# Kernel optimization log

Hardware: AMD Instinct MI355X
Metric: run time of the kernel (lower is better)

Reference implementation:

```python
import jax, jax.numpy as jnp
import numpy as np

D_MODEL = 528
N_HEADS = 16
FEAT = 16           # feature_dim
HEAD_DIM = 33       # d_model // num_heads == 2*FEAT + 1 (required by the module's math)
WINDOW = 64
EPS = 1e-9


def setup_inputs() -> dict:
    key = jax.random.key(0)
    ks = jax.random.split(key, 10)
    B, S = 2, 2048
    hidden_states = jax.random.normal(ks[0], (B, S, D_MODEL), dtype=jnp.float32)
    attention_mask = jnp.ones((B, S), dtype=jnp.int32)
    sc = 0.02
    # weights stored as (in, out); torch Linear applies x @ W.T so this is the transposed weight
    Wq_lin = jax.random.normal(ks[1], (D_MODEL, FEAT * N_HEADS), dtype=jnp.float32) * sc
    Wk_lin = jax.random.normal(ks[2], (D_MODEL, FEAT * N_HEADS), dtype=jnp.float32) * sc
    Wv_lin = jax.random.normal(ks[3], (D_MODEL, HEAD_DIM * N_HEADS), dtype=jnp.float32) * sc
    Wo_lin = jax.random.normal(ks[4], (HEAD_DIM * N_HEADS, D_MODEL), dtype=jnp.float32) * sc
    Wq_win = jax.random.normal(ks[5], (D_MODEL, D_MODEL), dtype=jnp.float32) * sc
    Wk_win = jax.random.normal(ks[6], (D_MODEL, D_MODEL), dtype=jnp.float32) * sc
    Wv_win = jax.random.normal(ks[7], (D_MODEL, D_MODEL), dtype=jnp.float32) * sc
    Wo_win = jax.random.normal(ks[8], (D_MODEL, D_MODEL), dtype=jnp.float32) * sc
    return {
        "hidden_states": hidden_states,
        "attention_mask": attention_mask,
        "Wq_lin": Wq_lin, "Wk_lin": Wk_lin, "Wv_lin": Wv_lin, "Wo_lin": Wo_lin,
        "Wq_win": Wq_win, "Wk_win": Wk_win, "Wv_win": Wv_win, "Wo_win": Wo_win,
    }


def _linear_attention(x, mask, Wq, Wk, Wv, Wo):
    B, S, _ = x.shape
    q = (x @ Wq).reshape(B, S, N_HEADS, FEAT).transpose(0, 2, 1, 3)      # bhsf
    k = (x @ Wk).reshape(B, S, N_HEADS, FEAT).transpose(0, 2, 1, 3)
    v = (x @ Wv).reshape(B, S, N_HEADS, HEAD_DIM).transpose(0, 2, 1, 3)  # bhse
    # Taylor feature map: [1, q, 0.5*q^2] -> feature dim 2*FEAT+1 == HEAD_DIM
    qe = jnp.concatenate([jnp.ones_like(q[..., :1]), q, 0.5 * q * q], axis=-1)
    ke = jnp.concatenate([jnp.ones_like(k[..., :1]), k, 0.5 * k * k], axis=-1)
    kv = jnp.einsum('bhnd,bhne->bhde', ke, v)          # (B,H,Dexp,HEAD_DIM)
    qkv = jnp.einsum('bhnd,bhde->bhne', qe, kv)        # (B,H,S,HEAD_DIM)
    # z[b,h,n,e] = (sum_d qe[b,h,n,d]) * ksum[b,h,e]  (faithful to torch einsum with size-1 n)
    z = qe.sum(-1, keepdims=True) * ke.sum(2, keepdims=True)  # (B,H,S,Dexp==HEAD_DIM)
    out = qkv / (z + EPS)
    out = jnp.where((mask == 0)[:, None, :, None], 0.0, out)
    out = out.transpose(0, 2, 1, 3).reshape(B, S, N_HEADS * HEAD_DIM)
    return out @ Wo


def _window_attention(x, mask, Wq, Wk, Wv, Wo):
    B, S, _ = x.shape
    q = (x @ Wq).reshape(B, S, N_HEADS, HEAD_DIM).transpose(0, 2, 1, 3)
    k = (x @ Wk).reshape(B, S, N_HEADS, HEAD_DIM).transpose(0, 2, 1, 3)
    v = (x @ Wv).reshape(B, S, N_HEADS, HEAD_DIM).transpose(0, 2, 1, 3)
    scores = jnp.einsum('bhnd,bhmd->bhnm', q, k) / np.sqrt(HEAD_DIM).astype(np.float32)
    # tril(diagonal=window_size-1): allow key index m <= n + WINDOW - 1
    i = jnp.arange(S)[:, None]
    j = jnp.arange(S)[None, :]
    band = (j <= i + WINDOW - 1)
    neg_inf = jnp.asarray(-jnp.inf, scores.dtype)
    scores = jnp.where(band[None, None], scores, neg_inf)
    scores = jnp.where((mask == 0)[:, None, None, :], neg_inf, scores)
    attn = jax.nn.softmax(scores, axis=-1)
    out = jnp.einsum('bhnm,bhmd->bhnd', attn, v)
    out = out.transpose(0, 2, 1, 3).reshape(B, S, D_MODEL)
    return out @ Wo


def reference(hidden_states, attention_mask,
              Wq_lin, Wk_lin, Wv_lin, Wo_lin,
              Wq_win, Wk_win, Wv_win, Wo_win):
    lin = _linear_attention(hidden_states, attention_mask, Wq_lin, Wk_lin, Wv_lin, Wo_lin)
    win = _window_attention(hidden_states, attention_mask, Wq_win, Wk_win, Wv_win, Wo_win)
    return lin + win
```

## Files before the change

kernel.cpp:

```cpp
#include <hip/hip_runtime.h>

#define NH 16
#define FEAT 16
#define HD 33
#define DM 528
#define WIN 64
#define EPSF 1e-9f
#define K1C (0.17407765595569785f * 1.4426950408889634f)
#define KP 544
#define KSPLIT 1632
#define NPROJ 2112
#define KOUT 1056
#define OPS 4352
#define NCH 16
#define ZPARTS 4

typedef float f32x4 __attribute__((ext_vector_type(4)));
typedef short short8 __attribute__((ext_vector_type(8)));

__device__ inline ushort f2bf(float f) {
  uint u = __float_as_uint(f);
  uint r = u + 0x7fffu + ((u >> 16) & 1u);
  return (ushort)(r >> 16);
}
__device__ inline ushort f2bf_tr(float f) { return (ushort)(__float_as_uint(f) >> 16); }
__device__ inline float bf2f(ushort u) { return __uint_as_float(((uint)u) << 16); }

__global__ __launch_bounds__(256) void prep_all(const float* __restrict__ x,
                                                const float* __restrict__ Wq_lin,
                                                const float* __restrict__ Wk_lin,
                                                const float* __restrict__ Wv_lin,
                                                const float* __restrict__ Wo_lin,
                                                const float* __restrict__ Wq_win,
                                                const float* __restrict__ Wk_win,
                                                const float* __restrict__ Wv_win,
                                                const float* __restrict__ Wo_win,
                                                ushort* __restrict__ xhi,
                                                ushort* __restrict__ xlo,
                                                ushort* __restrict__ Wqks,
                                                ushort* __restrict__ WprojT,
                                                ushort* __restrict__ WoT2, int M) {
  const int stride = gridDim.x * 256;
  const int tid0 = blockIdx.x * 256 + threadIdx.x;
  for (int j = tid0; j < M * 68; j += stride) {
    int row = j / 68, c8 = (j - row * 68) * 8;
    short8 h8, l8;
    if (c8 < DM) {
      float4 f0 = *(const float4*)&x[(size_t)row * DM + c8];
      float4 f1 = *(const float4*)&x[(size_t)row * DM + c8 + 4];
      float vv[8] = {f0.x, f0.y, f0.z, f0.w, f1.x, f1.y, f1.z, f1.w};
#pragma unroll
      for (int z = 0; z < 8; ++z) {
        ushort h = f2bf(vv[z]);
        h8[z] = (short)h;
        l8[z] = (short)f2bf(vv[z] - bf2f(h));
      }
    } else {
      h8 = (short8){0, 0, 0, 0, 0, 0, 0, 0};
      l8 = h8;
    }
    *(short8*)&xhi[(size_t)row * KP + c8] = h8;
    *(short8*)&xlo[(size_t)row * KP + c8] = l8;
  }
  for (int i = tid0; i < 512 * KSPLIT; i += stride) {
    int n = i / KSPLIT, kp = i - n * KSPLIT;
    int seg = kp / KP, kk = kp - seg * KP;
    float v = 0.f;
    if (kk < DM) v = (n < 256) ? Wq_lin[(size_t)kk * 256 + n] : Wk_lin[(size_t)kk * 256 + (n - 256)];
    ushort h = f2bf(v);
    if (seg == 2) h = f2bf(v - bf2f(h));
    Wqks[i] = h;
  }
  for (int i = tid0; i < NPROJ * KP; i += stride) {
    int n = i / KP, k = i - n * KP;
    float v = 0.f;
    if (k < DM) {
      if (n < DM) v = Wq_win[(size_t)k * DM + n];
      else if (n < 2 * DM) v = Wk_win[(size_t)k * DM + (n - DM)] * K1C;
      else if (n < 3 * DM) v = Wv_win[(size_t)k * DM + (n - 2 * DM)];
      else v = Wv_lin[(size_t)k * DM + (n - 3 * DM)];
    }
    WprojT[i] = f2bf(v);
  }
  for (int i = tid0; i < DM * KOUT; i += stride) {
    int n = i / KOUT, k = i - n * KOUT;
    float v = (k < DM) ? Wo_lin[(size_t)k * DM + n] : Wo_win[(size_t)(k - DM) * DM + n];
    WoT2[i] = f2bf(v);
  }
}

__global__ __launch_bounds__(256) void proj_fused(const ushort* __restrict__ xhi,
                                                  const ushort* __restrict__ xlo,
                                                  const ushort* __restrict__ Wqks,
                                                  const ushort* __restrict__ WprojT,
                                                  float* __restrict__ qk,
                                                  ushort* __restrict__ qkvw,
                                                  float* __restrict__ v_lin,
                                                  const int* __restrict__ maskp,
                                                  int S) {
  __shared__ ushort As[128][36];
  __shared__ ushort Bs[128][36];
  const int bm = blockIdx.x * 128;
  const int tid = threadIdx.x;
  const int lane = tid & 63, w = tid >> 6;
  const int lo = lane & 15, hi = lane >> 4;
  const int wr = w >> 1, wc = w & 1;
  const short8 zv = {0, 0, 0, 0, 0, 0, 0, 0};
  f32x4 acc[4][4];
#pragma unroll
  for (int mb = 0; mb < 4; ++mb)
#pragma unroll
    for (int nb = 0; nb < 4; ++nb) acc[mb][nb] = (f32x4){0.f, 0.f, 0.f, 0.f};

  if (blockIdx.y < 17) {
    const int bn = blockIdx.y * 128;
    for (int k0 = 0; k0 < KP; k0 += 32) {
      short8 a_ld[2], b_ld[2];
#pragma unroll
      for (int p = 0; p < 2; ++p) {
        int c = tid + p * 256;
        int row = c >> 2, cc = c & 3;
        a_ld[p] = *(const short8*)&xhi[(size_t)(bm + row) * KP + k0 + cc * 8];
        int bnr = bn + row;
        b_ld[p] = (bnr < NPROJ) ? *(const short8*)&WprojT[(size_t)bnr * KP + k0 + cc * 8] : zv;
      }
      __syncthreads();
#pragma unroll
      for (int p = 0; p < 2; ++p) {
        int c = tid + p * 256;
        int row = c >> 2, cc = c & 3;
        *(short8*)&As[row][cc * 8] = a_ld[p];
        *(short8*)&Bs[row][cc * 8] = b_ld[p];
      }
      __syncthreads();
      short8 afr[4], bfr[4];
#pragma unroll
      for (int mb = 0; mb < 4; ++mb) afr[mb] = *(const short8*)&As[wr * 64 + 16 * mb + lo][8 * hi];
#pragma unroll
      for (int nb = 0; nb < 4; ++nb) bfr[nb] = *(const short8*)&Bs[wc * 64 + 16 * nb + lo][8 * hi];
#pragma unroll
      for (int mb = 0; mb < 4; ++mb)
#pragma unroll
        for (int nb = 0; nb < 4; ++nb)
          acc[mb][nb] = __builtin_amdgcn_mfma_f32_16x16x32_bf16(afr[mb], bfr[nb], acc[mb][nb], 0, 0, 0);
    }
#pragma unroll
    for (int nb = 0; nb < 4; ++nb) {
      const int col = bn + wc * 64 + 16 * nb + lo;
      if (col >= NPROJ) continue;
      const int seg = col / DM;
      const int cc = col - seg * DM;
      if (seg == 3) {
#pragma unroll
        for (int mb = 0; mb < 4; ++mb)
#pragma unroll
          for (int r = 0; r < 4; ++r) {
            int row = bm + wr * 64 + 16 * mb + 4 * hi + r;
            v_lin[(size_t)row * DM + cc] = acc[mb][nb][r];
          }
      } else {
        const uint h = ((uint)cc * 993u) >> 15;
        const int e = cc - (int)h * 33;
        ushort* dst = qkvw + (size_t)seg * (32u * (uint)S * 40u);
#pragma unroll
        for (int mb = 0; mb < 4; ++mb)
#pragma unroll
          for (int r = 0; r < 4; ++r) {
            int row = bm + wr * 64 + 16 * mb + 4 * hi + r;
            int b = (row >= S) ? 1 : 0;
            int nn = row - b * S;
            float val = acc[mb][nb][r];
            if (seg == 2) {
              size_t tb = (size_t)(b * NH + (int)h) * 40;
              dst[(tb + e) * S + nn] = f2bf(val);
              if (e == 0) {
                dst[(tb + 33) * S + nn] = 0x3F80;
#pragma unroll
                for (int z = 34; z < 40; ++z) dst[(tb + z) * S + nn] = 0;
              }
            } else {
              size_t base = ((size_t)(b * NH + (int)h) * S + nn) * 40;
              dst[base + e] = f2bf(val);
              if (e == 0) {
                ushort pad33 = (seg == 0) ? (ushort)0x3F80
                                          : (maskp[row] ? (ushort)0 : f2bf(-1e30f));
                dst[base + 33] = pad33;
#pragma unroll
                for (int z = 34; z < 40; ++z) dst[base + z] = 0;
              }
            }
          }
      }
    }
  } else {
    const int bn = (blockIdx.y - 17) * 128;
    for (int k0 = 0; k0 < KSPLIT; k0 += 32) {
      const int seg = k0 / KP;
      const int kk = k0 - seg * KP;
      const ushort* xsrc = (seg == 1) ? xlo : xhi;
      short8 a_ld[2], b_ld[2];
#pragma unroll
      for (int p = 0; p < 2; ++p) {
        int c = tid + p * 256;
        int row = c >> 2, cc = c & 3;
        a_ld[p] = *(const short8*)&xsrc[(size_t)(bm + row) * KP + kk + cc * 8];
        b_ld[p] = *(const short8*)&Wqks[(size_t)(bn + row) * KSPLIT + k0 + cc * 8];
      }
      __syncthreads();
#pragma unroll
      for (int p = 0; p < 2; ++p) {
        int c = tid + p * 256;
        int row = c >> 2, cc = c & 3;
        *(short8*)&As[row][cc * 8] = a_ld[p];
        *(short8*)&Bs[row][cc * 8] = b_ld[p];
      }
      __syncthreads();
      short8 afr[4], bfr[4];
#pragma unroll
      for (int mb = 0; mb < 4; ++mb) afr[mb] = *(const short8*)&As[wr * 64 + 16 * mb + lo][8 * hi];
#pragma unroll
      for (int nb = 0; nb < 4; ++nb) bfr[nb] = *(const short8*)&Bs[wc * 64 + 16 * nb + lo][8 * hi];
#pragma unroll
      for (int mb = 0; mb < 4; ++mb)
#pragma unroll
        for (int nb = 0; nb < 4; ++nb)
          acc[mb][nb] = __builtin_amdgcn_mfma_f32_16x16x32_bf16(afr[mb], bfr[nb], acc[mb][nb], 0, 0, 0);
    }
#pragma unroll
    for (int mb = 0; mb < 4; ++mb)
#pragma unroll
      for (int nb = 0; nb < 4; ++nb) {
        int col = bn + wc * 64 + 16 * nb + lo;
#pragma unroll
        for (int r = 0; r < 4; ++r) {
          int row = bm + wr * 64 + 16 * mb + 4 * hi + r;
          qk[(size_t)row * 512 + col] = acc[mb][nb][r];
        }
      }
  }
}

__global__ __launch_bounds__(256) void gemm_out(const ushort* __restrict__ A,
                                                const ushort* __restrict__ Bt,
                                                float* __restrict__ C, int S) {
  __shared__ ushort As[128][36];
  __shared__ ushort Bs[128][36];
  const int bm = blockIdx.x * 128, bn = blockIdx.y * 128;
  const int tid = threadIdx.x;
  const int lane = tid & 63, w = tid >> 6;
  const int lo = lane & 15, hi = lane >> 4;
  const int wr = w >> 1, wc = w & 1;
  f32x4 acc[4][4];
#pragma unroll
  for (int mb = 0; mb < 4; ++mb)
#pragma unroll
    for (int nb = 0; nb < 4; ++nb) acc[mb][nb] = (f32x4){0.f, 0.f, 0.f, 0.f};
  const short8 zv = {0, 0, 0, 0, 0, 0, 0, 0};

  for (int k0 = 0; k0 < KOUT; k0 += 32) {
    short8 a_ld[2], b_ld[2];
#pragma unroll
    for (int p = 0; p < 2; ++p) {
      int c = tid + p * 256;
      int row = c >> 2, cc = c & 3;
      a_ld[p] = *(const short8*)&A[(size_t)(bm + row) * KOUT + k0 + cc * 8];
      int bnr = bn + row;
      b_ld[p] = (bnr < DM) ? *(const short8*)&Bt[(size_t)bnr * KOUT + k0 + cc * 8] : zv;
    }
    __syncthreads();
#pragma unroll
    for (int p = 0; p < 2; ++p) {
      int c = tid + p * 256;
      int row = c >> 2, cc = c & 3;
      *(short8*)&As[row][cc * 8] = a_ld[p];
      *(short8*)&Bs[row][cc * 8] = b_ld[p];
    }
    __syncthreads();
    short8 afr[4], bfr[4];
#pragma unroll
    for (int mb = 0; mb < 4; ++mb) afr[mb] = *(const short8*)&As[wr * 64 + 16 * mb + lo][8 * hi];
#pragma unroll
    for (int nb = 0; nb < 4; ++nb) bfr[nb] = *(const short8*)&Bs[wc * 64 + 16 * nb + lo][8 * hi];
#pragma unroll
    for (int mb = 0; mb < 4; ++mb)
#pragma unroll
      for (int nb = 0; nb < 4; ++nb)
        acc[mb][nb] = __builtin_amdgcn_mfma_f32_16x16x32_bf16(afr[mb], bfr[nb], acc[mb][nb], 0, 0, 0);
  }
#pragma unroll
  for (int nb = 0; nb < 4; ++nb) {
    const int col = bn + wc * 64 + 16 * nb + lo;
    if (col >= DM) continue;
#pragma unroll
    for (int mb = 0; mb < 4; ++mb)
#pragma unroll
      for (int r = 0; r < 4; ++r) {
        int row = bm + wr * 64 + 16 * mb + 4 * hi + r;
        C[(size_t)row * DM + col] = acc[mb][nb][r];
      }
  }
}

__global__ __launch_bounds__(256) void lin_kv_part(const float* __restrict__ qk,
                                                   const float* __restrict__ v_lin,
                                                   float* __restrict__ kvp,
                                                   int B, int S) {
  const int bh = blockIdx.x, chunk = blockIdx.y;
  const int b = bh >> 4, h = bh & 15;
  const int tid = threadIdx.x;
  __shared__ float kraw[64][17];
  __shared__ float vsh[64][36];
  if (tid < 64) { vsh[tid][33] = 1.f; vsh[tid][34] = 0.f; vsh[tid][35] = 0.f; }
  f32x4 acc0 = {0.f, 0.f, 0.f, 0.f}, acc1 = {0.f, 0.f, 0.f, 0.f};
  const int d0 = tid / 9, c40 = (tid % 9) * 4;
  const int idx1 = tid + 256;
  const int d1 = idx1 / 9, c41 = (idx1 % 9) * 4;
  const int SC = S / NCH;
  const int nbeg = chunk * SC;
  __syncthreads();
  for (int n0 = nbeg; n0 < nbeg + SC; n0 += 64) {
    {
      int row = tid >> 2, f4 = (tid & 3) * 4;
      float4 kv4 = *(const float4*)&qk[(size_t)(b * S + n0 + row) * 512 + 256 + h * 16 + f4];
      kraw[row][f4 + 0] = kv4.x; kraw[row][f4 + 1] = kv4.y;
      kraw[row][f4 + 2] = kv4.z; kraw[row][f4 + 3] = kv4.w;
    }
    for (int i = tid; i < 64 * 33; i += 256) {
      int n = i / 33, e = i - n * 33;
      vsh[n][e] = v_lin[(size_t)(b * S + n0 + n) * DM + h * HD + e];
    }
    __syncthreads();
#pragma unroll 4
    for (int n = 0; n < 64; ++n) {
      {
        float ke;
        if (d0 == 0) ke = 1.f;
        else if (d0 < 17) ke = kraw[n][d0 - 1];
        else { float kk = kraw[n][d0 - 17]; ke = 0.5f * kk * kk; }
        f32x4 v = *(const f32x4*)&vsh[n][c40];
        acc0 += ke * v;
      }
      if (idx1 < 297) {
        float ke;
        if (d1 < 17) ke = kraw[n][d1 - 1];
        else { float kk = kraw[n][d1 - 17]; ke = 0.5f * kk * kk; }
        f32x4 v = *(const f32x4*)&vsh[n][c41];
        acc1 += ke * v;
      }
    }
    __syncthreads();
  }
  float* dst = kvp + (size_t)(bh * NCH + chunk) * 1188;
  *(f32x4*)&dst[d0 * 36 + c40] = acc0;
  if (idx1 < 297) *(f32x4*)&dst[d1 * 36 + c41] = acc1;
}

__global__ __launch_bounds__(256) void lin_red(const float* __restrict__ kvp,
                                               float* __restrict__ kvr) {
  int bh = blockIdx.x;
  for (int i = threadIdx.x; i < 1188; i += 256) {
    float s = 0.f;
#pragma unroll
    for (int c = 0; c < NCH; ++c) s += kvp[(size_t)(bh * NCH + c) * 1188 + i];
    kvr[(size_t)bh * 1188 + i] = s;
  }
}

__global__ __launch_bounds__(256) void win_lin(const ushort* __restrict__ qwb,
                                               const ushort* __restrict__ kwb,
                                               const ushort* __restrict__ vwbT,
                                               ushort* __restrict__ Opart,
                                               const float* __restrict__ qk,
                                               const float* __restrict__ kvr,
                                               const int* __restrict__ mask,
                                               ushort* __restrict__ cat,
                                               int B, int S, int NT2) {
  __shared__ ushort Ps[4][32][72];
  const int tid = threadIdx.x;
  const int NWINBLK = NT2 * 32 * ZPARTS;
  const int bx = blockIdx.x;

  if (bx < NWINBLK) {
    const int part = bx / (NT2 * 32);
    const int rem = bx - part * (NT2 * 32);
    const int bh = rem / NT2;
    const int qt = NT2 - 1 - (rem - bh * NT2);
    const int NT = NT2 * 2;
    const int T = min(NT, 2 * qt + 3);
    if (part >= T) return;
    const int n0 = qt * 128;
    const int lane = tid & 63, w = tid >> 6;
    const int lo = lane & 15, hi = lane >> 4;
    const short8 zv = {0, 0, 0, 0, 0, 0, 0, 0};

    short8 qf[2][2];
#pragma unroll
    for (int qr = 0; qr < 2; ++qr) {
      const ushort* qrow = qwb + ((size_t)bh * S + n0 + w * 32 + qr * 16 + lo) * 40;
      qf[qr][0] = *(const short8*)&qrow[8 * hi];
      qf[qr][1] = (hi == 0) ? *(const short8*)&qrow[32] : zv;
    }

    const ushort* kb = kwb + (size_t)bh * S * 40;
    const ushort* vb = vwbT + (size_t)bh * 40 * S;
    int evc[3];
#pragma unroll
    for (int eb = 0; eb < 3; ++eb) {
      int e = 16 * eb + lo;
      evc[eb] = (e > 39) ? 39 : e;
    }

    f32x4 Oacc[2][3];
#pragma unroll
    for (int qr = 0; qr < 2; ++qr)
#pragma unroll
      for (int eb = 0; eb < 3; ++eb) Oacc[qr][eb] = (f32x4){0.f, 0.f, 0.f, 0.f};

    for (int t = part; t < T; t += ZPARTS) {
      const int m0 = t * 64;
      short8 kf0[4], kf1[4];
#pragma unroll
      for (int bb = 0; bb < 4; ++bb) {
        const ushort* kr = kb + (size_t)(m0 + 16 * bb + lo) * 40;
        kf0[bb] = *(const short8*)&kr[8 * hi];
        kf1[bb] = *(const short8*)&kr[32];
      }
      short8 vf0[3], vf1[3];
#pragma unroll
      for (int eb = 0; eb < 3; ++eb) {
        const ushort* vr = vb + (size_t)evc[eb] * S + m0;
        vf0[eb] = *(const short8*)&vr[8 * hi];
        vf1[eb] = *(const short8*)&vr[32 + 8 * hi];
      }

      f32x4 accS[2][4];
#pragma unroll
      for (int qr = 0; qr < 2; ++qr)
#pragma unroll
        for (int bb = 0; bb < 4; ++bb) accS[qr][bb] = (f32x4){0.f, 0.f, 0.f, 0.f};
      __builtin_amdgcn_s_setprio(1);
#pragma unroll
      for (int bb = 0; bb < 4; ++bb)
#pragma unroll
        for (int qr = 0; qr < 2; ++qr) {
          accS[qr][bb] = __builtin_amdgcn_mfma_f32_16x16x32_bf16(qf[qr][0], kf0[bb], accS[qr][bb], 0, 0, 0);
          accS[qr][bb] = __builtin_amdgcn_mfma_f32_16x16x32_bf16(qf[qr][1], kf1[bb], accS[qr][bb], 0, 0, 0);
        }
      __builtin_amdgcn_s_setprio(0);

      const bool boundary = (m0 > n0);
      const int dmn = m0 - n0;
#pragma unroll
      for (int qr = 0; qr < 2; ++qr)
#pragma unroll
        for (int bb = 0; bb < 4; ++bb)
#pragma unroll
          for (int r = 0; r < 4; ++r) {
            float p = exp2f(accS[qr][bb][r]);
            if (boundary) {
              int rr = w * 32 + qr * 16 + 4 * hi + r;
              int c = 16 * bb + lo;
              if (c > rr + 63 - dmn) p = 0.f;
            }
            Ps[w][qr * 16 + 4 * hi + r][16 * bb + lo] = f2bf_tr(p);
          }

      __builtin_amdgcn_s_setprio(1);
#pragma unroll
      for (int qr = 0; qr < 2; ++qr) {
        short8 pf0 = *(const short8*)&Ps[w][qr * 16 + lo][8 * hi];
        short8 pf1 = *(const short8*)&Ps[w][qr * 16 + lo][32 + 8 * hi];
#pragma unroll
        for (int eb = 0; eb < 3; ++eb) {
          Oacc[qr][eb] = __builtin_amdgcn_mfma_f32_16x16x32_bf16(pf0, vf0[eb], Oacc[qr][eb], 0, 0, 0);
          Oacc[qr][eb] = __builtin_amdgcn_mfma_f32_16x16x32_bf16(pf1, vf1[eb], Oacc[qr][eb], 0, 0, 0);
        }
      }
      __builtin_amdgcn_s_setprio(0);
    }

    const size_t ob = ((size_t)(bh * NT2 + qt) * ZPARTS + part) * OPS;
#pragma unroll
    for (int qr = 0; qr < 2; ++qr)
#pragma unroll
      for (int eb = 0; eb < 3; ++eb) {
        int e = 16 * eb + lo;
        if (e < 34) {
#pragma unroll
          for (int r = 0; r < 4; ++r)
            Opart[ob + (size_t)(w * 32 + qr * 16 + 4 * hi + r) * 34 + e] = f2bf(Oacc[qr][eb][r]);
        }
      }
  } else {
    const int bs = bx - NWINBLK;
    const int b = (bs >= S) ? 1 : 0;
    float* qsh = (float*)Ps;
    for (int i = tid; i < NH * FEAT; i += 256)
      qsh[(i >> 4) * 17 + (i & 15)] = qk[(size_t)bs * 512 + i];
    __syncthreads();
    const int msk = mask[bs];
    for (int o = tid; o < DM; o += 256) {
      uint h = ((uint)o * 993u) >> 15;
      int e = o - (int)h * 33;
      const float* kvh = kvr + (size_t)(b * NH + (int)h) * 1188;
      float qsum = 1.f, qkv = kvh[e];
#pragma unroll
      for (int f = 0; f < FEAT; ++f) {
        float q = qsh[h * 17 + f];
        float q2 = 0.5f * q * q;
        qsum += q + q2;
        qkv += q * kvh[(1 + f) * 36 + e] + q2 * kvh[(17 + f) * 36 + e];
      }
      float z = qsum * kvh[e * 36 + 33];
      float outv = qkv / (z + EPSF);
      if (msk == 0) outv = 0.f;
      cat[(size_t)bs * KOUT + o] = f2bf(outv);
    }
  }
}

__global__ __launch_bounds__(256) void win_combine(const ushort* __restrict__ Opart,
                                                   ushort* __restrict__ cat,
                                                   int S, int NT2) {
  const int qt = blockIdx.x, bh = blockIdx.y;
  const int b = bh >> 4, h = bh & 15;
  const int T = min(NT2 * 2, 2 * qt + 3);
  const int P = min(ZPARTS, T);
  const size_t base = (size_t)(bh * NT2 + qt) * ZPARTS * OPS;
  __shared__ float linv[128];
  const int tid = threadIdx.x;
  if (tid < 128) {
    float l = 0.f;
    for (int p = 0; p < P; ++p) l += bf2f(Opart[base + (size_t)p * OPS + tid * 34 + 33]);
    linv[tid] = (l > 0.f) ? 1.f / l : 0.f;
  }
  __syncthreads();
  for (int i = tid; i < 128 * 33; i += 256) {
    int row = i / 33, e = i - row * 33;
    float o = 0.f;
    for (int p = 0; p < P; ++p) o += bf2f(Opart[base + (size_t)p * OPS + row * 34 + e]);
    int n = qt * 128 + row;
    cat[((size_t)(b * S + n)) * KOUT + DM + h * HD + e] = f2bf(o * linv[row]);
  }
}

extern "C" void kernel_launch(void* const* d_in, const int* in_sizes, int n_in,
                              void* d_out, int out_size, void* d_ws, size_t ws_size,
                              hipStream_t stream) {
  const float* x      = (const float*)d_in[0];
  const int*   mask   = (const int*)d_in[1];
  const float* Wq_lin = (const float*)d_in[2];
  const float* Wk_lin = (const float*)d_in[3];
  const float* Wv_lin = (const float*)d_in[4];
  const float* Wo_lin = (const float*)d_in[5];
  const float* Wq_win = (const float*)d_in[6];
  const float* Wk_win = (const float*)d_in[7];
  const float* Wv_win = (const float*)d_in[8];
  const float* Wo_win = (const float*)d_in[9];
  float* out = (float*)d_out;

  const int BS = in_sizes[1];
  const int B = 2;
  const int S = BS / B;
  const int NT2 = S / 128;
  const int M = BS;

  float* ws = (float*)d_ws;
  float* qk      = ws;  ws += (size_t)BS * 512;
  float* v_lin   = ws;  ws += (size_t)BS * DM;
  float* kvp     = ws;  ws += (size_t)B * NH * NCH * 1188;
  float* kvr     = ws;  ws += (size_t)B * NH * 1188;
  ushort* ub     = (ushort*)ws;
  ushort* x_hi   = ub;  ub += (size_t)M * KP;
  ushort* x_lo   = ub;  ub += (size_t)M * KP;
  ushort* qkvw   = ub;  ub += (size_t)3 * 32 * S * 40;
  ushort* cat    = ub;  ub += (size_t)M * KOUT;
  ushort* WprojT = ub;  ub += (size_t)NPROJ * KP;
  ushort* WoT2   = ub;  ub += (size_t)DM * KOUT;
  ushort* Wqks   = ub;  ub += (size_t)512 * KSPLIT;
  ushort* Opart  = ub;  ub += (size_t)32 * NT2 * ZPARTS * OPS;

  ushort* qwb  = qkvw;
  ushort* kwb  = qkvw + (size_t)32 * S * 40;
  ushort* vwbT = qkvw + (size_t)64 * S * 40;

  dim3 blk(256);

  prep_all<<<2048, blk, 0, stream>>>(x, Wq_lin, Wk_lin, Wv_lin, Wo_lin,
                                     Wq_win, Wk_win, Wv_win, Wo_win,
                                     x_hi, x_lo, Wqks, WprojT, WoT2, M);

  proj_fused<<<dim3(M / 128, 21), blk, 0, stream>>>(x_hi, x_lo, Wqks, WprojT,
                                                    qk, qkvw, v_lin, mask, S);

  lin_kv_part<<<dim3(B * NH, NCH), blk, 0, stream>>>(qk, v_lin, kvp, B, S);
  lin_red<<<dim3(B * NH), blk, 0, stream>>>(kvp, kvr);

  win_lin<<<dim3(NT2 * 32 * ZPARTS + BS), blk, 0, stream>>>(
      qwb, kwb, vwbT, Opart, qk, kvr, mask, cat, B, S, NT2);

  win_combine<<<dim3(NT2, B * NH), blk, 0, stream>>>(Opart, cat, S, NT2);

  gemm_out<<<dim3(M / 128, (DM + 127) / 128), blk, 0, stream>>>(cat, WoT2, out, S);
}
```

Before: 222.0 us.

## Regroup kernels: fuse window attention with kv partials, combine with linear output

Moves the linear-attention kv partial computation into the same launch as the windowed attention blocks, and merges the window combine step with the per-token linear-attention output into one launch. This cuts the launch count and lets independent work share the GPU instead of running as small serial kernels. Block indexing is remapped so bh is the fastest-varying index. The kv-partial blocks reuse the window kernel's shared memory, and the combine kernel adds a second shared array. The price is mixed block types with different runtimes inside one grid.

```diff
diff --git a/kernel.cpp b/kernel.cpp
--- a/kernel.cpp
+++ b/kernel.cpp
@@ -301,60 +301,6 @@
   }
 }
 
-__global__ __launch_bounds__(256) void lin_kv_part(const float* __restrict__ qk,
-                                                   const float* __restrict__ v_lin,
-                                                   float* __restrict__ kvp,
-                                                   int B, int S) {
-  const int bh = blockIdx.x, chunk = blockIdx.y;
-  const int b = bh >> 4, h = bh & 15;
-  const int tid = threadIdx.x;
-  __shared__ float kraw[64][17];
-  __shared__ float vsh[64][36];
-  if (tid < 64) { vsh[tid][33] = 1.f; vsh[tid][34] = 0.f; vsh[tid][35] = 0.f; }
-  f32x4 acc0 = {0.f, 0.f, 0.f, 0.f}, acc1 = {0.f, 0.f, 0.f, 0.f};
-  const int d0 = tid / 9, c40 = (tid % 9) * 4;
-  const int idx1 = tid + 256;
-  const int d1 = idx1 / 9, c41 = (idx1 % 9) * 4;
-  const int SC = S / NCH;
-  const int nbeg = chunk * SC;
-  __syncthreads();
-  for (int n0 = nbeg; n0 < nbeg + SC; n0 += 64) {
-    {
-      int row = tid >> 2, f4 = (tid & 3) * 4;
-      float4 kv4 = *(const float4*)&qk[(size_t)(b * S + n0 + row) * 512 + 256 + h * 16 + f4];
-      kraw[row][f4 + 0] = kv4.x; kraw[row][f4 + 1] = kv4.y;
-      kraw[row][f4 + 2] = kv4.z; kraw[row][f4 + 3] = kv4.w;
-    }
-    for (int i = tid; i < 64 * 33; i += 256) {
-      int n = i / 33, e = i - n * 33;
-      vsh[n][e] = v_lin[(size_t)(b * S + n0 + n) * DM + h * HD + e];
-    }
-    __syncthreads();
-#pragma unroll 4
-    for (int n = 0; n < 64; ++n) {
-      {
-        float ke;
-        if (d0 == 0) ke = 1.f;
-        else if (d0 < 17) ke = kraw[n][d0 - 1];
-        else { float kk = kraw[n][d0 - 17]; ke = 0.5f * kk * kk; }
-        f32x4 v = *(const f32x4*)&vsh[n][c40];
-        acc0 += ke * v;
-      }
-      if (idx1 < 297) {
-        float ke;
-        if (d1 < 17) ke = kraw[n][d1 - 1];
-        else { float kk = kraw[n][d1 - 17]; ke = 0.5f * kk * kk; }
-        f32x4 v = *(const f32x4*)&vsh[n][c41];
-        acc1 += ke * v;
-      }
-    }
-    __syncthreads();
-  }
-  float* dst = kvp + (size_t)(bh * NCH + chunk) * 1188;
-  *(f32x4*)&dst[d0 * 36 + c40] = acc0;
-  if (idx1 < 297) *(f32x4*)&dst[d1 * 36 + c41] = acc1;
-}
-
 __global__ __launch_bounds__(256) void lin_red(const float* __restrict__ kvp,
                                                float* __restrict__ kvr) {
   int bh = blockIdx.x;
@@ -366,25 +312,24 @@
   }
 }
 
-__global__ __launch_bounds__(256) void win_lin(const ushort* __restrict__ qwb,
-                                               const ushort* __restrict__ kwb,
-                                               const ushort* __restrict__ vwbT,
-                                               ushort* __restrict__ Opart,
-                                               const float* __restrict__ qk,
-                                               const float* __restrict__ kvr,
-                                               const int* __restrict__ mask,
-                                               ushort* __restrict__ cat,
-                                               int B, int S, int NT2) {
-  __shared__ ushort Ps[4][32][72];
+__global__ __launch_bounds__(256) void win_kv(const ushort* __restrict__ qwb,
+                                              const ushort* __restrict__ kwb,
+                                              const ushort* __restrict__ vwbT,
+                                              ushort* __restrict__ Opart,
+                                              const float* __restrict__ qk,
+                                              const float* __restrict__ v_lin,
+                                              float* __restrict__ kvp,
+                                              int B, int S, int NT2) {
+  __shared__ ushort sh[4][32][72];
   const int tid = threadIdx.x;
   const int NWINBLK = NT2 * 32 * ZPARTS;
   const int bx = blockIdx.x;
 
   if (bx < NWINBLK) {
-    const int part = bx / (NT2 * 32);
-    const int rem = bx - part * (NT2 * 32);
-    const int bh = rem / NT2;
-    const int qt = NT2 - 1 - (rem - bh * NT2);
+    const int bh = bx & 31;
+    const int qp = bx >> 5;
+    const int part = qp / NT2;
+    const int qt = NT2 - 1 - (qp - part * NT2);
     const int NT = NT2 * 2;
     const int T = min(NT, 2 * qt + 3);
     if (part >= T) return;
@@ -392,6 +337,7 @@
     const int lane = tid & 63, w = tid >> 6;
     const int lo = lane & 15, hi = lane >> 4;
     const short8 zv = {0, 0, 0, 0, 0, 0, 0, 0};
+    ushort (*Ps)[32][72] = sh;
 
     short8 qf[2][2];
 #pragma unroll
@@ -492,9 +438,95 @@
         }
       }
   } else {
-    const int bs = bx - NWINBLK;
+    const int idx = bx - NWINBLK;
+    const int bh = idx & 31, chunk = idx >> 5;
+    const int b = bh >> 4, h = bh & 15;
+    float* kraw = (float*)sh;
+    float* vsh = kraw + 64 * 17;
+    if (tid < 64) { vsh[tid * 36 + 33] = 1.f; vsh[tid * 36 + 34] = 0.f; vsh[tid * 36 + 35] = 0.f; }
+    f32x4 acc0 = {0.f, 0.f, 0.f, 0.f}, acc1 = {0.f, 0.f, 0.f, 0.f};
+    const int d0 = tid / 9, c40 = (tid % 9) * 4;
+    const int idx1 = tid + 256;
+    const int d1 = idx1 / 9, c41 = (idx1 % 9) * 4;
+    const int SC = S / NCH;
+    const int nbeg = chunk * SC;
+    __syncthreads();
+    for (int n0 = nbeg; n0 < nbeg + SC; n0 += 64) {
+      {
+        int row = tid >> 2, f4 = (tid & 3) * 4;
+        float4 kv4 = *(const float4*)&qk[(size_t)(b * S + n0 + row) * 512 + 256 + h * 16 + f4];
+        kraw[row * 17 + f4 + 0] = kv4.x; kraw[row * 17 + f4 + 1] = kv4.y;
+        kraw[row * 17 + f4 + 2] = kv4.z; kraw[row * 17 + f4 + 3] = kv4.w;
+      }
+      for (int i = tid; i < 64 * 33; i += 256) {
+        int n = i / 33, e = i - n * 33;
+        vsh[n * 36 + e] = v_lin[(size_t)(b * S + n0 + n) * DM + h * HD + e];
+      }
+      __syncthreads();
+#pragma unroll 4
+      for (int n = 0; n < 64; ++n) {
+        {
+          float ke;
+          if (d0 == 0) ke = 1.f;
+          else if (d0 < 17) ke = kraw[n * 17 + d0 - 1];
+          else { float kk = kraw[n * 17 + d0 - 17]; ke = 0.5f * kk * kk; }
+          f32x4 v = *(const f32x4*)&vsh[n * 36 + c40];
+          acc0 += ke * v;
+        }
+        if (idx1 < 297) {
+          float ke;
+          if (d1 < 17) ke = kraw[n * 17 + d1 - 1];
+          else { float kk = kraw[n * 17 + d1 - 17]; ke = 0.5f * kk * kk; }
+          f32x4 v = *(const f32x4*)&vsh[n * 36 + c41];
+          acc1 += ke * v;
+        }
+      }
+      __syncthreads();
+    }
+    float* dst = kvp + (size_t)(bh * NCH + chunk) * 1188;
+    *(f32x4*)&dst[d0 * 36 + c40] = acc0;
+    if (idx1 < 297) *(f32x4*)&dst[d1 * 36 + c41] = acc1;
+  }
+}
+
+__global__ __launch_bounds__(256) void comb_lin(const ushort* __restrict__ Opart,
+                                                const float* __restrict__ qk,
+                                                const float* __restrict__ kvr,
+                                                const int* __restrict__ mask,
+                                                ushort* __restrict__ cat,
+                                                int B, int S, int NT2) {
+  __shared__ float shf[160];
+  const int tid = threadIdx.x;
+  const int NCOMB = NT2 * 32;
+  const int bx = blockIdx.x;
+
+  if (bx < NCOMB) {
+    const int bh = bx & 31;
+    const int qt = bx >> 5;
+    const int b = bh >> 4, h = bh & 15;
+    const int T = min(NT2 * 2, 2 * qt + 3);
+    const int P = min(ZPARTS, T);
+    const size_t base = (size_t)(bh * NT2 + qt) * ZPARTS * OPS;
+    float* linv = shf;
+    if (tid < 128) {
+      float l = 0.f;
+      for (int p = 0; p < P; ++p) l += bf2f(Opart[base + (size_t)p * OPS + tid * 34 + 33]);
+      linv[tid] = (l > 0.f) ? 1.f / l : 0.f;
+    }
+    __syncthreads();
+    for (int i = tid; i < 128 * 33; i += 256) {
+      int row = i / 33, e = i - row * 33;
+      float o = 0.f;
+      for (int p = 0; p < P; ++p) o += bf2f(Opart[base + (size_t)p * OPS + row * 34 + e]);
+      int n = qt * 128 + row;
+      cat[((size_t)(b * S + n)) * KOUT + DM + h * HD + e] = f2bf(o * linv[row]);
+    }
+  } else {
+    const int bs = bx - NCOMB;
     const int b = (bs >= S) ? 1 : 0;
-    float* qsh = (float*)Ps;
+    float* qsh = shf;
+    __shared__ float qsh2[NH * 17];
+    qsh = qsh2;
     for (int i = tid; i < NH * FEAT; i += 256)
       qsh[(i >> 4) * 17 + (i & 15)] = qk[(size_t)bs * 512 + i];
     __syncthreads();
@@ -516,31 +548,6 @@
       if (msk == 0) outv = 0.f;
       cat[(size_t)bs * KOUT + o] = f2bf(outv);
     }
-  }
-}
-
-__global__ __launch_bounds__(256) void win_combine(const ushort* __restrict__ Opart,
-                                                   ushort* __restrict__ cat,
-                                                   int S, int NT2) {
-  const int qt = blockIdx.x, bh = blockIdx.y;
-  const int b = bh >> 4, h = bh & 15;
-  const int T = min(NT2 * 2, 2 * qt + 3);
-  const int P = min(ZPARTS, T);
-  const size_t base = (size_t)(bh * NT2 + qt) * ZPARTS * OPS;
-  __shared__ float linv[128];
-  const int tid = threadIdx.x;
-  if (tid < 128) {
-    float l = 0.f;
-    for (int p = 0; p < P; ++p) l += bf2f(Opart[base + (size_t)p * OPS + tid * 34 + 33]);
-    linv[tid] = (l > 0.f) ? 1.f / l : 0.f;
-  }
-  __syncthreads();
-  for (int i = tid; i < 128 * 33; i += 256) {
-    int row = i / 33, e = i - row * 33;
-    float o = 0.f;
-    for (int p = 0; p < P; ++p) o += bf2f(Opart[base + (size_t)p * OPS + row * 34 + e]);
-    int n = qt * 128 + row;
-    cat[((size_t)(b * S + n)) * KOUT + DM + h * HD + e] = f2bf(o * linv[row]);
   }
 }
 
@@ -593,13 +600,12 @@
   proj_fused<<<dim3(M / 128, 21), blk, 0, stream>>>(x_hi, x_lo, Wqks, WprojT,
                                                     qk, qkvw, v_lin, mask, S);
 
-  lin_kv_part<<<dim3(B * NH, NCH), blk, 0, stream>>>(qk, v_lin, kvp, B, S);
+  win_kv<<<dim3(NT2 * 32 * ZPARTS + B * NH * NCH), blk, 0, stream>>>(
+      qwb, kwb, vwbT, Opart, qk, v_lin, kvp, B, S, NT2);
+
   lin_red<<<dim3(B * NH), blk, 0, stream>>>(kvp, kvr);
 
-  win_lin<<<dim3(NT2 * 32 * ZPARTS + BS), blk, 0, stream>>>(
-      qwb, kwb, vwbT, Opart, qk, kvr, mask, cat, B, S, NT2);
-
-  win_combine<<<dim3(NT2, B * NH), blk, 0, stream>>>(Opart, cat, S, NT2);
+  comb_lin<<<dim3(NT2 * 32 + BS), blk, 0, stream>>>(Opart, qk, kvr, mask, cat, B, S, NT2);
 
   gemm_out<<<dim3(M / 128, (DM + 127) / 128), blk, 0, stream>>>(cat, WoT2, out, S);
 }
```

New measurement: 193.1 us. 1.15x faster.
